# Performance work log

Hardware: AMD Instinct MI355X
Metric: run time of the kernel (lower is better)

Reference implementation:

```python
import jax, jax.numpy as jnp
import numpy as np

PAD = 2
EPS = 1e-5


def setup_inputs() -> dict:
    key = jax.random.key(0)
    k1, = jax.random.split(key, 1)
    N, C, H, W = 32, 64, 224, 224
    x = jax.random.normal(k1, (N, C, H, W), dtype=jnp.float32)
    bn_weight = jnp.ones((C,), dtype=jnp.float32)
    bn_bias = jnp.zeros((C,), dtype=jnp.float32)
    post_scale = jnp.asarray(0.5, dtype=jnp.float32)
    return {"x": x, "bn_weight": bn_weight, "bn_bias": bn_bias, "post_scale": post_scale}


def reference(x, bn_weight, bn_bias, post_scale):
    # 1) reflection pad H and W by PAD on each side -> (N, C, H+2p, W+2p)
    pad_x = jnp.pad(x, ((0, 0), (0, 0), (PAD, PAD), (PAD, PAD)), mode="reflect")
    # 2-4) GLU over [pad_x, roll(pad_x)] along channels == pad_x * sigmoid(roll)
    pad_x_roll = jnp.roll(pad_x, shift=1, axis=1)
    gated = pad_x * jax.nn.sigmoid(pad_x_roll)
    # 5) global average pool -> (N, C)
    pooled = gated.mean(axis=(2, 3))
    # 6) BatchNorm1d (training mode: batch stats, biased variance, affine)
    mu = pooled.mean(axis=0)
    var = pooled.var(axis=0)  # biased, matches BN normalization
    normed = (pooled - mu) / jnp.sqrt(var + EPS) * bn_weight + bn_bias
    # 7-9) sigmoid reweight + channel-mean residual + scalar scale + exact GELU
    scale = jax.nn.sigmoid(normed)[:, :, None, None]
    channel_mean = pad_x.mean(axis=(2, 3), keepdims=True)
    out = jax.nn.gelu((gated * scale + channel_mean) * post_scale, approximate=False)
    return out.reshape(out.shape[0], -1)
```

## Files before the change

### kernel.cpp

```cpp
#include <hip/hip_runtime.h>
#include <math.h>

#define NB 32
#define CB 64
#define HH 224
#define WW 224
#define PADP 2
#define HP (HH + 2*PADP)
#define WP (WW + 2*PADP)
#define HW (HH*WW)
#define HWP (HP*WP)
#define EPSV 1e-5f
#define CHUNKS 49

__device__ __forceinline__ float fsig(float v) {
    float e = __expf(-v);
    return __builtin_amdgcn_rcpf(1.0f + e);
}
__device__ __forceinline__ float fgelu(float v) {
    float t = v * (1.5957691216f + 0.0713548162f * v * v);
    return v * fsig(t);
}

__global__ __launch_bounds__(256) void k_pool2(const float* __restrict__ x,
                                               float* __restrict__ partG,
                                               float* __restrict__ partX) {
    int b = blockIdx.x;
    int n = b / CHUNKS;
    int chunk = b - n * CHUNKS;
    int tid = threadIdx.x;
    int i = chunk * 1024 + tid * 4;
    int h  = i / WW;
    int w0 = i - h * WW;
    float wh = 1.0f + (float)((h == 1) | (h == 2) | (h == HH-3) | (h == HH-2));
    float w_0 = wh * (1.0f + (float)((w0   == 1) | (w0   == 2) | (w0   == WW-3) | (w0   == WW-2)));
    float w_1 = wh * (1.0f + (float)((w0+1 == 1) | (w0+1 == 2) | (w0+1 == WW-3) | (w0+1 == WW-2)));
    float w_2 = wh * (1.0f + (float)((w0+2 == 1) | (w0+2 == 2) | (w0+2 == WW-3) | (w0+2 == WW-2)));
    float w_3 = wh * (1.0f + (float)((w0+3 == 1) | (w0+3 == 2) | (w0+3 == WW-3) | (w0+3 == WW-2)));

    const float* xn = x + (size_t)n * CB * HW;
    float4 prev = *(const float4*)(xn + (size_t)(CB-1) * HW + i);

    __shared__ float lds[CB][8];
    int wave = tid >> 6, lane = tid & 63;

    for (int c = 0; c < CB; ++c) {
        float4 cur = *(const float4*)(xn + (size_t)c * HW + i);
        float sG = w_0 * cur.x * fsig(prev.x)
                 + w_1 * cur.y * fsig(prev.y)
                 + w_2 * cur.z * fsig(prev.z)
                 + w_3 * cur.w * fsig(prev.w);
        float sX = w_0 * cur.x + w_1 * cur.y + w_2 * cur.z + w_3 * cur.w;
        for (int off = 32; off >= 1; off >>= 1) {
            sG += __shfl_xor(sG, off);
            sX += __shfl_xor(sX, off);
        }
        if (lane == 0) { lds[c][wave * 2] = sG; lds[c][wave * 2 + 1] = sX; }
        prev = cur;
    }
    __syncthreads();
    if (tid < 128) {
        int c = tid >> 1, v = tid & 1;
        float s = lds[c][v] + lds[c][2 + v] + lds[c][4 + v] + lds[c][6 + v];
        size_t idx = ((size_t)n * CB + c) * CHUNKS + chunk;
        if (v == 0) partG[idx] = s; else partX[idx] = s;
    }
}

__global__ __launch_bounds__(64) void k_red(const float* __restrict__ partG,
                                            const float* __restrict__ partX,
                                            float* __restrict__ pooled,
                                            float* __restrict__ cmean) {
    int bc = blockIdx.x;
    int t = threadIdx.x;
    float g = 0.f, xx = 0.f;
    if (t < CHUNKS) {
        g  = partG[(size_t)bc * CHUNKS + t];
        xx = partX[(size_t)bc * CHUNKS + t];
    }
    for (int off = 32; off >= 1; off >>= 1) {
        g  += __shfl_xor(g, off);
        xx += __shfl_xor(xx, off);
    }
    if (t == 0) {
        pooled[bc] = g  * (1.0f / (float)HWP);
        cmean[bc]  = xx * (1.0f / (float)HWP);
    }
}

__global__ __launch_bounds__(64) void k_bn(const float* __restrict__ pooled,
                                           const float* __restrict__ bnw,
                                           const float* __restrict__ bnb,
                                           float* __restrict__ scale) {
    int c = blockIdx.x;
    int t = threadIdx.x;
    float v = 0.f;
    if (t < 32) v = pooled[t * CB + c];
    float s = v;
    for (int off = 16; off >= 1; off >>= 1) s += __shfl_xor(s, off);
    float mu = s * (1.0f / 32.0f);
    float d = v - mu;
    float q = d * d;
    for (int off = 16; off >= 1; off >>= 1) q += __shfl_xor(q, off);
    float var = q * (1.0f / 32.0f);
    if (t < 32) {
        float normed = d * rsqrtf(var + EPSV) * bnw[c] + bnb[c];
        scale[t * CB + c] = 1.0f / (1.0f + expf(-normed));
    }
}

__global__ __launch_bounds__(256) void k_out(const float* __restrict__ x,
                                             const float* __restrict__ scale,
                                             const float* __restrict__ cmean,
                                             const float* __restrict__ post_scale,
                                             float* __restrict__ out) {
    int b  = blockIdx.x;
    int n  = b / HP;
    int hp = b - n * HP;
    int rh = hp - PADP; rh = rh < 0 ? -rh : (rh >= HH ? 2*HH - 2 - rh : rh);
    int wave = threadIdx.x >> 6;
    int lane = threadIdx.x & 63;
    bool act = lane < 56;
    float ps = post_scale[0];

    const float* xrow = x + (size_t)n * CB * HW + (size_t)rh * WW;
    const float* sc_row = scale + n * CB;
    const float* cm_row = cmean + n * CB;

    int c0 = wave * 16;
    int cg = (c0 + CB - 1) & (CB - 1);
    float4 prev = make_float4(0.f, 0.f, 0.f, 0.f);
    if (act) prev = *(const float4*)(xrow + (size_t)cg * HW + 4 * lane);

    for (int k = 0; k < 16; ++k) {
        int c = c0 + k;
        float4 cur = make_float4(0.f, 0.f, 0.f, 0.f);
        if (act) cur = *(const float4*)(xrow + (size_t)c * HW + 4 * lane);
        float scp = sc_row[c] * ps;
        float cmp = cm_row[c] * ps;
        float o0 = fgelu(fmaf(cur.x * fsig(prev.x), scp, cmp));
        float o1 = fgelu(fmaf(cur.y * fsig(prev.y), scp, cmp));
        float o2 = fgelu(fmaf(cur.z * fsig(prev.z), scp, cmp));
        float o3 = fgelu(fmaf(cur.w * fsig(prev.w), scp, cmp));
        float* orow = out + ((size_t)n * CB + c) * HWP + (size_t)hp * WP;
        if (act) {
            *(float2*)(orow + 4 * lane + 2) = make_float2(o0, o1);
            *(float2*)(orow + 4 * lane + 4) = make_float2(o2, o3);
            if (lane == 0)  *(float2*)(orow)       = make_float2(o2, o1);
            if (lane == 55) *(float2*)(orow + 226) = make_float2(o2, o1);
        }
        prev = cur;
    }
}

extern "C" void kernel_launch(void* const* d_in, const int* in_sizes, int n_in,
                              void* d_out, int out_size, void* d_ws, size_t ws_size,
                              hipStream_t stream) {
    const float* x   = (const float*)d_in[0];
    const float* bnw = (const float*)d_in[1];
    const float* bnb = (const float*)d_in[2];
    const float* ps  = (const float*)d_in[3];
    float* out = (float*)d_out;

    size_t npart = (size_t)NB * CB * CHUNKS;
    float* partG  = (float*)d_ws;
    float* partX  = partG + npart;
    float* pooled = partX + npart;
    float* cmean  = pooled + NB * CB;
    float* scale  = cmean  + NB * CB;

    k_pool2<<<NB * CHUNKS, 256, 0, stream>>>(x, partG, partX);
    k_red<<<NB * CB, 64, 0, stream>>>(partG, partX, pooled, cmean);
    k_bn<<<CB, 64, 0, stream>>>(pooled, bnw, bnb, scale);
    k_out<<<NB * HP, 256, 0, stream>>>(x, scale, cmean, ps, out);
}
```

Baseline: 283.1 us.

## Split pooling channels across waves and use aligned nontemporal float4 output stores

The pooling kernel now gives each wave its own 16-channel slice, with every lane covering four float4 positions, instead of all waves walking all 64 channels. This removes the LDS reduction and the block barrier, and puts more independent loads in flight per thread. The output kernel shuffles neighbouring lane values so each lane writes one aligned 16-byte nontemporal store, replacing two misaligned float2 stores plus edge stores. The cost is more registers per thread in pooling and extra cross-lane shuffles in the output kernel.

```diff
diff --git a/kernel.cpp b/kernel.cpp
--- a/kernel.cpp
+++ b/kernel.cpp
@@ -13,6 +13,8 @@
 #define EPSV 1e-5f
 #define CHUNKS 49
 
+typedef float v4f __attribute__((ext_vector_type(4)));
+
 __device__ __forceinline__ float fsig(float v) {
     float e = __expf(-v);
     return __builtin_amdgcn_rcpf(1.0f + e);
@@ -21,49 +23,68 @@
     float t = v * (1.5957691216f + 0.0713548162f * v * v);
     return v * fsig(t);
 }
-
-__global__ __launch_bounds__(256) void k_pool2(const float* __restrict__ x,
+__device__ __forceinline__ float edgew(int w) {
+    return 1.0f + (float)((w == 1) | (w == 2) | (w == WW-3) | (w == WW-2));
+}
+
+__global__ __launch_bounds__(256) void k_pool3(const float* __restrict__ x,
                                                float* __restrict__ partG,
                                                float* __restrict__ partX) {
     int b = blockIdx.x;
     int n = b / CHUNKS;
     int chunk = b - n * CHUNKS;
-    int tid = threadIdx.x;
-    int i = chunk * 1024 + tid * 4;
-    int h  = i / WW;
-    int w0 = i - h * WW;
-    float wh = 1.0f + (float)((h == 1) | (h == 2) | (h == HH-3) | (h == HH-2));
-    float w_0 = wh * (1.0f + (float)((w0   == 1) | (w0   == 2) | (w0   == WW-3) | (w0   == WW-2)));
-    float w_1 = wh * (1.0f + (float)((w0+1 == 1) | (w0+1 == 2) | (w0+1 == WW-3) | (w0+1 == WW-2)));
-    float w_2 = wh * (1.0f + (float)((w0+2 == 1) | (w0+2 == 2) | (w0+2 == WW-3) | (w0+2 == WW-2)));
-    float w_3 = wh * (1.0f + (float)((w0+3 == 1) | (w0+3 == 2) | (w0+3 == WW-3) | (w0+3 == WW-2)));
+    int wave = threadIdx.x >> 6;
+    int lane = threadIdx.x & 63;
+
+    int p0 = chunk * 1024 + lane * 4;
+    float4 wgt[4];
+    #pragma unroll
+    for (int m = 0; m < 4; ++m) {
+        int pm = p0 + m * 256;
+        int h  = pm / WW;
+        int w0 = pm - h * WW;
+        float wh = 1.0f + (float)((h == 1) | (h == 2) | (h == HH-3) | (h == HH-2));
+        wgt[m].x = wh * edgew(w0);
+        wgt[m].y = wh * edgew(w0 + 1);
+        wgt[m].z = wh * edgew(w0 + 2);
+        wgt[m].w = wh * edgew(w0 + 3);
+    }
 
     const float* xn = x + (size_t)n * CB * HW;
-    float4 prev = *(const float4*)(xn + (size_t)(CB-1) * HW + i);
-
-    __shared__ float lds[CB][8];
-    int wave = tid >> 6, lane = tid & 63;
-
-    for (int c = 0; c < CB; ++c) {
-        float4 cur = *(const float4*)(xn + (size_t)c * HW + i);
-        float sG = w_0 * cur.x * fsig(prev.x)
-                 + w_1 * cur.y * fsig(prev.y)
-                 + w_2 * cur.z * fsig(prev.z)
-                 + w_3 * cur.w * fsig(prev.w);
-        float sX = w_0 * cur.x + w_1 * cur.y + w_2 * cur.z + w_3 * cur.w;
+    int c0 = wave * 16;
+    int cg = (c0 + CB - 1) & (CB - 1);
+    float4 prev[4];
+    #pragma unroll
+    for (int m = 0; m < 4; ++m)
+        prev[m] = *(const float4*)(xn + (size_t)cg * HW + p0 + m * 256);
+
+    for (int k = 0; k < 16; ++k) {
+        int c = c0 + k;
+        float4 cur[4];
+        #pragma unroll
+        for (int m = 0; m < 4; ++m)
+            cur[m] = *(const float4*)(xn + (size_t)c * HW + p0 + m * 256);
+        float sG = 0.f, sX = 0.f;
+        #pragma unroll
+        for (int m = 0; m < 4; ++m) {
+            sG += wgt[m].x * cur[m].x * fsig(prev[m].x);
+            sG += wgt[m].y * cur[m].y * fsig(prev[m].y);
+            sG += wgt[m].z * cur[m].z * fsig(prev[m].z);
+            sG += wgt[m].w * cur[m].w * fsig(prev[m].w);
+            sX += wgt[m].x * cur[m].x + wgt[m].y * cur[m].y
+                + wgt[m].z * cur[m].z + wgt[m].w * cur[m].w;
+            prev[m] = cur[m];
+        }
+        #pragma unroll
         for (int off = 32; off >= 1; off >>= 1) {
             sG += __shfl_xor(sG, off);
             sX += __shfl_xor(sX, off);
         }
-        if (lane == 0) { lds[c][wave * 2] = sG; lds[c][wave * 2 + 1] = sX; }
-        prev = cur;
-    }
-    __syncthreads();
-    if (tid < 128) {
-        int c = tid >> 1, v = tid & 1;
-        float s = lds[c][v] + lds[c][2 + v] + lds[c][4 + v] + lds[c][6 + v];
-        size_t idx = ((size_t)n * CB + c) * CHUNKS + chunk;
-        if (v == 0) partG[idx] = s; else partX[idx] = s;
+        if (lane == 0) {
+            size_t idx = ((size_t)n * CB + c) * CHUNKS + chunk;
+            partG[idx] = sG;
+            partX[idx] = sX;
+        }
     }
 }
 
@@ -142,12 +163,15 @@
         float o1 = fgelu(fmaf(cur.y * fsig(prev.y), scp, cmp));
         float o2 = fgelu(fmaf(cur.z * fsig(prev.z), scp, cmp));
         float o3 = fgelu(fmaf(cur.w * fsig(prev.w), scp, cmp));
-        float* orow = out + ((size_t)n * CB + c) * HWP + (size_t)hp * WP;
-        if (act) {
-            *(float2*)(orow + 4 * lane + 2) = make_float2(o0, o1);
-            *(float2*)(orow + 4 * lane + 4) = make_float2(o2, o3);
-            if (lane == 0)  *(float2*)(orow)       = make_float2(o2, o1);
-            if (lane == 55) *(float2*)(orow + 226) = make_float2(o2, o1);
+        float o1s = __shfl(o1, lane - 1);
+        float o2s = __shfl(o2, lane - 1);
+        float o3s = __shfl(o3, lane - 1);
+        v4f st = { o2s, o3s, o0, o1 };
+        if (lane == 0)  st = (v4f){ o2, o1, o0, o1 };
+        if (lane == 56) st = (v4f){ o2s, o3s, o2s, o1s };
+        if (lane < 57) {
+            float* orow = out + ((size_t)n * CB + c) * HWP + (size_t)hp * WP;
+            __builtin_nontemporal_store(st, (v4f*)(orow + 4 * lane));
         }
         prev = cur;
     }
@@ -169,7 +193,7 @@
     float* cmean  = pooled + NB * CB;
     float* scale  = cmean  + NB * CB;
 
-    k_pool2<<<NB * CHUNKS, 256, 0, stream>>>(x, partG, partX);
+    k_pool3<<<NB * CHUNKS, 256, 0, stream>>>(x, partG, partX);
     k_red<<<NB * CB, 64, 0, stream>>>(partG, partX, pooled, cmean);
     k_bn<<<CB, 64, 0, stream>>>(pooled, bnw, bnb, scale);
     k_out<<<NB * HP, 256, 0, stream>>>(x, scale, cmean, ps, out);
```

Result: faster. 272.5 us (-3.7%).
